# Optimization experiments

Hardware: AMD Instinct MI355X
Metric: run time of the kernel (lower is better)

Reference implementation:

```python
import jax, jax.numpy as jnp
import numpy as np

CONF_THRES = 0.25
IOU_THRES = 0.45
MAX_WH = 4096.0   # class offset for class-aware NMS (nc=1 -> offset is 0 anyway)
K = 1024          # fixed candidate pool (jit-friendly stand-in for max_nms)
MAX_DET = 300     # max detections per image (as in yolov5 NMS)


def xywh2xyxy(b):
    xy, wh = b[..., :2], b[..., 2:4]
    return jnp.concatenate([xy - wh * 0.5, xy + wh * 0.5], axis=-1)


def box_iou(a, b):
    # a: [K,4], b: [K,4] in xyxy -> [K,K] IoU
    area_a = (a[:, 2] - a[:, 0]) * (a[:, 3] - a[:, 1])
    area_b = (b[:, 2] - b[:, 0]) * (b[:, 3] - b[:, 1])
    lt = jnp.maximum(a[:, None, :2], b[None, :, :2])
    rb = jnp.minimum(a[:, None, 2:], b[None, :, 2:])
    wh = jnp.clip(rb - lt, 0.0)
    inter = wh[..., 0] * wh[..., 1]
    return inter / (area_a[:, None] + area_b[None, :] - inter + 1e-9)


def _nms_single(pred):
    # pred: [N, 6] = [xywh, obj_conf, cls_conf] (single class)
    boxes = xywh2xyxy(pred[:, :4])
    conf = pred[:, 4] * pred[:, 5]          # obj * cls  (nc=1 best-class path)
    cls = jnp.zeros_like(conf)              # single class -> class 0
    scores = jnp.where(conf > CONF_THRES, conf, -1.0)  # conf filter
    top_scores, idx = jax.lax.top_k(scores, K)          # candidates, sorted desc
    b = boxes[idx]
    c = cls[idx]
    bo = b + (c * MAX_WH)[:, None]          # class offset (no-op for nc=1)
    iou = box_iou(bo, bo)                   # [K, K]
    valid = top_scores > CONF_THRES

    def body(i, keep):
        sup = (iou[i] > IOU_THRES) & keep[i] & (jnp.arange(K) > i)
        return keep & ~sup

    keep = jax.lax.fori_loop(0, K, body, valid)  # greedy suppression
    keep_scores = jnp.where(keep, top_scores, -1.0)
    _, sel = jax.lax.top_k(keep_scores, MAX_DET)  # top MAX_DET kept, score order
    det = jnp.concatenate([b, top_scores[:, None], c[:, None]], axis=-1)[sel]
    det_valid = keep_scores[sel] > CONF_THRES
    return jnp.where(det_valid[:, None], det, 0.0)  # [MAX_DET, 6], zero-padded


def setup_inputs() -> dict:
    key = jax.random.key(0)
    k1, k2, k3, k4 = jax.random.split(key, 4)
    B, N = 32, 25200
    xy = jax.random.uniform(k1, (B, N, 2), jnp.float32) * 640.0
    wh = jax.random.uniform(k2, (B, N, 2), jnp.float32) * 160.0 + 4.0
    obj = jax.random.uniform(k3, (B, N, 1), jnp.float32)
    clsc = jax.random.uniform(k4, (B, N, 1), jnp.float32)
    x = jnp.concatenate([xy, wh, obj, clsc], axis=-1)  # [B, N, 6]
    return {"x": x}


def reference(x):
    # NMS.forward: non_max_suppression(x[0], conf_thres=0.25, iou_thres=0.45)
    return jax.vmap(_nms_single)(x)  # [B, MAX_DET, 6] (x1,y1,x2,y2,conf,cls)
```

## Files before the change

kernel.cpp:

```cpp
#include <hip/hip_runtime.h>
#include <stdint.h>

#define NBOX 25200
#define BATCH 32
#define TOPK 1024
#define MAXDET 300
#define BINCAP 2048
#define SEGCAP 256
#define NSEG 64
#define CONF_T 0.25f
#define IOU_T 0.45f
#define KEY_BIAS 0x3E800001u

#define SEGS_OFF   0u
#define SEGCNT_OFF 4194304u
#define GHIST_OFF  4202496u
#define SORTED_OFF 4726784u
#define SBOX_OFF   4988928u
#define SAREA_OFF  5513216u
#define MASKS_OFF  5644288u
#define WS_NEED    7741440u

__device__ __forceinline__ float iou_of(float4 a, float ar_a, float4 bq, float ar_b) {
    float xx1 = fmaxf(a.x, bq.x);
    float yy1 = fmaxf(a.y, bq.y);
    float xx2 = fminf(a.z, bq.z);
    float yy2 = fminf(a.w, bq.w);
    float iw = fmaxf(xx2 - xx1, 0.0f);
    float ih = fmaxf(yy2 - yy1, 0.0f);
    float inter = iw * ih;
    return inter / (ar_a + ar_b - inter + 1e-9f);
}

__global__ __launch_bounds__(256) void k1_extract(const float* __restrict__ x,
                                                  unsigned long long* __restrict__ segs,
                                                  unsigned* __restrict__ segcnt,
                                                  unsigned* __restrict__ ghist) {
    const int blk = blockIdx.x;
    const int b = blk >> 4;
    const int sl = blk & 15;
    const int tid = threadIdx.x;
    const int lane = tid & 63;
    const int wv = tid >> 6;
    const int seg = sl * 4 + wv;
    const float* __restrict__ xb = x + (size_t)b * NBOX * 6;
    unsigned long long* __restrict__ sb = segs + ((size_t)b * NSEG + seg) * SEGCAP;

    __shared__ unsigned hist[256];
    hist[tid] = 0;
    __syncthreads();

    const int n0 = (seg * NBOX) / NSEG;
    const int n1 = ((seg + 1) * NBOX) / NSEG;
    unsigned base = 0;
    const unsigned long long lmask = (1ull << lane) - 1ull;
    #pragma unroll 2
    for (int n = n0 + lane; n < n1; n += 64) {
        float2 oc = *reinterpret_cast<const float2*>(xb + n * 6 + 4);
        float conf = oc.x * oc.y;
        bool take = conf > CONF_T;
        unsigned key = 0;
        if (take) {
            key = __float_as_uint(conf) - KEY_BIAS;
            atomicAdd(&hist[min(key >> 16, 255u)], 1u);
        }
        unsigned long long m = __ballot(take);
        if (take) {
            unsigned pos = base + (unsigned)__popcll(m & lmask);
            if (pos < SEGCAP)
                sb[pos] = ((unsigned long long)key << 32) | (unsigned)(~(unsigned)n);
        }
        base += (unsigned)__popcll(m);
    }
    if (lane == 0) segcnt[b * NSEG + seg] = min(base, (unsigned)SEGCAP);
    __syncthreads();
    ghist[(size_t)blk * 256 + tid] = hist[tid];
}

__global__ __launch_bounds__(1024) void k2_sort(const float* __restrict__ x,
                                                const unsigned long long* __restrict__ segs,
                                                const unsigned* __restrict__ segcnt,
                                                const unsigned* __restrict__ ghist,
                                                unsigned long long* __restrict__ sorted_g,
                                                float4* __restrict__ sbox,
                                                float* __restrict__ sarea) {
    const int b = blockIdx.x;
    const int tid = threadIdx.x;
    const int lane = tid & 63;
    const float* __restrict__ xb = x + (size_t)b * NBOX * 6;
    const unsigned long long* __restrict__ segs_b = segs + (size_t)b * NSEG * SEGCAP;

    __shared__ unsigned hist[256];
    __shared__ unsigned binstart[256];
    __shared__ unsigned bincnt[256];
    __shared__ int sh_selbin;
    __shared__ unsigned segcnt_l[NSEG];
    __shared__ unsigned long long cand[BINCAP];
    __shared__ unsigned long long sortedl[TOPK];

    if (tid < 256) {
        unsigned h = 0;
        #pragma unroll
        for (int sl = 0; sl < 16; ++sl) h += ghist[((size_t)(b * 16 + sl)) * 256 + tid];
        hist[tid] = h;
        bincnt[tid] = 0;
    }
    if (tid < NSEG) segcnt_l[tid] = segcnt[b * NSEG + tid];
    if (tid == 0) sh_selbin = 0;
    sortedl[tid] = 0ull;
    __syncthreads();

    if (tid < 64) {
        unsigned c0 = hist[tid*4+0], c1 = hist[tid*4+1];
        unsigned c2 = hist[tid*4+2], c3 = hist[tid*4+3];
        unsigned s3 = c3, s2 = c2 + s3, s1 = c1 + s2, s0 = c0 + s1;
        unsigned suf = s0;
        #pragma unroll
        for (int off = 1; off < 64; off <<= 1) {
            unsigned o = (unsigned)__shfl_down((int)suf, off);
            if (lane + off < 64) suf += o;
        }
        unsigned excl = suf - s0;
        binstart[tid*4+0] = excl + s1;
        binstart[tid*4+1] = excl + s2;
        binstart[tid*4+2] = excl + s3;
        binstart[tid*4+3] = excl;
        unsigned S0 = excl+s0, S1 = excl+s1, S2 = excl+s2, S3 = excl+s3;
        if (S0 >= TOPK && S1 < TOPK) sh_selbin = tid*4+0;
        if (S1 >= TOPK && S2 < TOPK) sh_selbin = tid*4+1;
        if (S2 >= TOPK && S3 < TOPK) sh_selbin = tid*4+2;
        if (S3 >= TOPK && excl < TOPK) sh_selbin = tid*4+3;
    }
    __syncthreads();
    const unsigned selbin = (unsigned)sh_selbin;
    const int C = (int)min(binstart[selbin] + hist[selbin], (unsigned)BINCAP);

    for (int idx = tid; idx < NSEG * SEGCAP; idx += 1024) {
        const int seg = idx >> 8;
        const int i = idx & (SEGCAP - 1);
        if (i < (int)segcnt_l[seg]) {
            unsigned long long pk = segs_b[idx];
            unsigned bin = (unsigned)(pk >> 48);
            if (bin >= selbin) {
                unsigned pos = binstart[bin] + atomicAdd(&bincnt[bin], 1u);
                if (pos < BINCAP) cand[pos] = pk;
            }
        }
    }
    __syncthreads();

    for (int e = tid; e < C; e += 1024) {
        unsigned long long mine = cand[e];
        unsigned bin = (unsigned)(mine >> 48);
        unsigned js = binstart[bin];
        unsigned je = min(js + hist[bin], (unsigned)C);
        int rank = (int)js;
        for (unsigned j = js; j < je; ++j) rank += (cand[j] > mine) ? 1 : 0;
        if (rank < TOPK) sortedl[rank] = mine;
    }
    __syncthreads();

    unsigned long long pk = sortedl[tid];
    sorted_g[(size_t)b * TOPK + tid] = pk;
    int n = (int)(~(unsigned)pk);
    if (n < 0 || n >= NBOX) n = 0;
    float2 p01 = *reinterpret_cast<const float2*>(xb + n * 6);
    float2 p23 = *reinterpret_cast<const float2*>(xb + n * 6 + 2);
    float x1 = p01.x - p23.x * 0.5f, y1 = p01.y - p23.y * 0.5f;
    float x2 = p01.x + p23.x * 0.5f, y2 = p01.y + p23.y * 0.5f;
    sbox[(size_t)b * TOPK + tid] = make_float4(x1, y1, x2, y2);
    sarea[(size_t)b * TOPK + tid] = (x2 - x1) * (y2 - y1);
}

__global__ __launch_bounds__(256) void k3_masks(const float4* __restrict__ sbox,
                                                const float* __restrict__ sarea,
                                                unsigned long long* __restrict__ masks) {
    const int b = blockIdx.y;
    const int wv = threadIdx.x >> 6;
    const int j = threadIdx.x & 63;
    const int p = blockIdx.x * 4 + wv;

    int jc = (int)((sqrtf(8.0f * (float)p + 1.0f) - 1.0f) * 0.5f);
    while ((jc + 1) * (jc + 2) / 2 <= p) ++jc;
    while (jc * (jc + 1) / 2 > p) --jc;
    const int ic = p - jc * (jc + 1) / 2;

    __shared__ float4 ibox[4][64];
    __shared__ float iar[4][64];
    ibox[wv][j] = sbox[(size_t)b * TOPK + ic * 64 + j];
    iar[wv][j]  = sarea[(size_t)b * TOPK + ic * 64 + j];
    const float4 mb = sbox[(size_t)b * TOPK + jc * 64 + j];
    const float ma  = sarea[(size_t)b * TOPK + jc * 64 + j];
    __syncthreads();

    unsigned long long w = 0ull;
    #pragma unroll 4
    for (int i = 0; i < 64; ++i) {
        float iou = iou_of(ibox[wv][i], iar[wv][i], mb, ma);
        bool bit = (iou > IOU_T) && (ic != jc || i < j);
        if (bit) w |= (1ull << i);
    }
    masks[(((size_t)b * 16 + jc) * 16 + ic) * 64 + j] = w;
}

__global__ __launch_bounds__(1024) void k4_resolve(const unsigned long long* __restrict__ sorted_g,
                                                   const float4* __restrict__ sbox,
                                                   const unsigned long long* __restrict__ masks,
                                                   float* __restrict__ out) {
    const int b = blockIdx.x;
    const int tid = threadIdx.x;
    const int lane = tid & 63;
    const int wv = tid >> 6;

    __shared__ unsigned long long keptb[16];
    __shared__ int pre[17];
    __shared__ int sh_acc, sh_cut;

    if (tid < 16) keptb[tid] = 0ull;
    if (tid == 0) { sh_acc = 0; sh_cut = 15; }

    const unsigned long long pk = sorted_g[(size_t)b * TOPK + tid];
    bool alive = (pk != 0ull);

    unsigned long long wcs[16];
    #pragma unroll
    for (int c = 0; c < 16; ++c)
        wcs[c] = masks[(((size_t)b * 16 + wv) * 16 + c) * 64 + lane];

    #pragma unroll
    for (int c = 0; c < 16; ++c) {
        if (wv == c) {
            unsigned long long rem = __ballot(alive);
            unsigned long long kept = 0ull;
            while (rem) {
                int i = __ffsll((long long)rem) - 1;
                unsigned long long bit = 1ull << i;
                kept |= bit;
                unsigned long long row = __ballot((unsigned)((wcs[c] >> i) & 1ull));
                rem &= ~(row | bit);
            }
            alive = (kept >> lane) & 1ull;
            if (lane == 0) {
                keptb[c] = kept;
                int acc = sh_acc + (int)__popcll(kept);
                sh_acc = acc;
                if (acc >= MAXDET && c < sh_cut) sh_cut = c;
            }
        }
        __syncthreads();
        if (c >= sh_cut) break;
        if (wv > c && alive && (wcs[c] & keptb[c])) alive = false;
    }

    if (tid == 0) {
        int acc = 0;
        #pragma unroll
        for (int c = 0; c < 16; ++c) { pre[c] = acc; acc += (int)__popcll(keptb[c]); }
        pre[16] = acc;
    }
    __syncthreads();
    const int total = pre[16];

    float* __restrict__ ob = out + (size_t)b * MAXDET * 6;
    const int rank = pre[wv] + (int)__popcll(keptb[wv] & ((1ull << lane) - 1ull));
    if (alive && wv <= sh_cut && rank < MAXDET) {
        float4 bx = sbox[(size_t)b * TOPK + tid];
        float sc_ = __uint_as_float((unsigned)(pk >> 32) + KEY_BIAS);
        ob[rank * 6 + 0] = bx.x;
        ob[rank * 6 + 1] = bx.y;
        ob[rank * 6 + 2] = bx.z;
        ob[rank * 6 + 3] = bx.w;
        ob[rank * 6 + 4] = sc_;
        ob[rank * 6 + 5] = 0.0f;
    }
    for (int r = tid; r < MAXDET; r += 1024) {
        if (r >= total) {
            #pragma unroll
            for (int cc = 0; cc < 6; ++cc) ob[r * 6 + cc] = 0.0f;
        }
    }
}

__global__ __launch_bounds__(1024) void nms_single_kernel(const float* __restrict__ x,
                                                          float* __restrict__ out) {
    const int b = blockIdx.x;
    const int tid = threadIdx.x;
    const int lane = tid & 63;
    const int wv = tid >> 6;
    const float* __restrict__ xb = x + (size_t)b * NBOX * 6;

    __shared__ unsigned hist[256];
    __shared__ int sh_selbin;
    __shared__ unsigned sh_cnt;
    __shared__ unsigned long long cand[BINCAP];
    __shared__ unsigned long long keys[TOPK];
    __shared__ float4 bbox[TOPK];
    __shared__ float bar[TOPK];
    __shared__ float4 lbox[2][64];
    __shared__ float lar[2][64];
    __shared__ int listn[2];
    __shared__ int wcnt[16], wpre[16];
    __shared__ int sh_total;

    if (tid < 256) hist[tid] = 0;
    if (tid == 0) { sh_selbin = 0; sh_cnt = 0; }
    keys[tid] = 0ull;
    __syncthreads();
    for (int n = tid; n < NBOX; n += 1024) {
        float2 oc = *reinterpret_cast<const float2*>(xb + n * 6 + 4);
        float conf = oc.x * oc.y;
        if (conf > CONF_T) atomicAdd(&hist[(__float_as_uint(conf) - KEY_BIAS) >> 16], 1u);
    }
    __syncthreads();
    if (tid < 64) {
        unsigned c0 = hist[tid*4+0], c1 = hist[tid*4+1];
        unsigned c2 = hist[tid*4+2], c3 = hist[tid*4+3];
        unsigned s3 = c3, s2 = c2 + s3, s1 = c1 + s2, s0 = c0 + s1;
        unsigned suf = s0;
        #pragma unroll
        for (int off = 1; off < 64; off <<= 1) {
            unsigned o = (unsigned)__shfl_down((int)suf, off);
            if (lane + off < 64) suf += o;
        }
        unsigned excl = suf - s0;
        unsigned S0 = excl+s0, S1 = excl+s1, S2 = excl+s2, S3 = excl+s3;
        if (S0 >= TOPK && S1 < TOPK) sh_selbin = tid*4+0;
        if (S1 >= TOPK && S2 < TOPK) sh_selbin = tid*4+1;
        if (S2 >= TOPK && S3 < TOPK) sh_selbin = tid*4+2;
        if (S3 >= TOPK && excl < TOPK) sh_selbin = tid*4+3;
    }
    __syncthreads();
    const unsigned selbin = (unsigned)sh_selbin;
    for (int n = tid; n < NBOX; n += 1024) {
        float2 oc = *reinterpret_cast<const float2*>(xb + n * 6 + 4);
        float conf = oc.x * oc.y;
        bool take = false; unsigned key = 0;
        if (conf > CONF_T) {
            key = __float_as_uint(conf) - KEY_BIAS;
            take = ((key >> 16) >= selbin);
        }
        unsigned long long m = __ballot(take);
        unsigned base = 0;
        if (lane == 0 && m) base = atomicAdd(&sh_cnt, (unsigned)__popcll(m));
        base = (unsigned)__shfl((int)base, 0);
        if (take) {
            unsigned pos = base + (unsigned)__popcll(m & ((1ull << lane) - 1ull));
            if (pos < BINCAP)
                cand[pos] = ((unsigned long long)key << 32) | (unsigned)(~(unsigned)n);
        }
    }
    __syncthreads();
    const int C = (int)min(sh_cnt, (unsigned)BINCAP);
    for (int e = tid; e < C; e += 1024) {
        unsigned long long mine = cand[e];
        int rank = 0;
        #pragma unroll 8
        for (int j = 0; j < C; ++j) rank += (cand[j] > mine) ? 1 : 0;
        if (rank < TOPK) keys[rank] = mine;
    }
    __syncthreads();
    unsigned long long kk = keys[tid];
    unsigned key24 = (unsigned)(kk >> 32);
    int n = (int)(~(unsigned)kk);
    bool alive = (kk != 0ull);
    if (n < 0 || n >= NBOX) { n = 0; alive = false; }
    float sc_ = __uint_as_float(key24 + KEY_BIAS);
    float2 p01 = *reinterpret_cast<const float2*>(xb + n * 6);
    float2 p23 = *reinterpret_cast<const float2*>(xb + n * 6 + 2);
    float x1 = p01.x - p23.x * 0.5f, y1 = p01.y - p23.y * 0.5f;
    float x2 = p01.x + p23.x * 0.5f, y2 = p01.y + p23.y * 0.5f;
    float4 mybox = make_float4(x1, y1, x2, y2);
    float my_ar = (x2 - x1) * (y2 - y1);
    bbox[tid] = mybox;
    bar[tid] = my_ar;
    __syncthreads();
    const int cbase = tid & ~63;
    unsigned long long my_mask = 0ull;
    #pragma unroll 4
    for (int i = 0; i < 64; ++i) {
        float iou = iou_of(bbox[cbase + i], bar[cbase + i], mybox, my_ar);
        if (i < lane && iou > IOU_T) my_mask |= (1ull << i);
    }
    for (int c = 0; c < 16; ++c) {
        if (c > 0 && wv >= c && alive) {
            const int pb = (c - 1) & 1;
            const int m = listn[pb];
            bool sup = false;
            #pragma unroll 2
            for (int t = 0; t < m; ++t) {
                float iou = iou_of(lbox[pb][t], lar[pb][t], mybox, my_ar);
                sup = sup || (iou > IOU_T);
            }
            alive = !sup;
        }
        if (wv == c) {
            unsigned long long rem = __ballot(alive);
            unsigned long long kept = 0ull;
            while (rem) {
                int i = __ffsll((long long)rem) - 1;
                unsigned long long bit = 1ull << i;
                kept |= bit;
                unsigned long long row = __ballot((unsigned)((my_mask >> i) & 1ull));
                rem &= ~(row | bit);
            }
            alive = (kept >> lane) & 1ull;
            int nk = __popcll(kept);
            int rk = __popcll(kept & ((1ull << lane) - 1ull));
            if (alive) { lbox[c & 1][rk] = mybox; lar[c & 1][rk] = my_ar; }
            if (lane == 0) listn[c & 1] = nk;
        }
        __syncthreads();
    }
    unsigned long long m = __ballot(alive);
    if (lane == 0) wcnt[wv] = __popcll(m);
    __syncthreads();
    if (tid == 0) {
        int acc = 0;
        for (int w2 = 0; w2 < 16; ++w2) { wpre[w2] = acc; acc += wcnt[w2]; }
        sh_total = acc;
    }
    __syncthreads();
    const int rank = wpre[wv] + (int)__popcll(m & ((1ull << lane) - 1ull));
    const int total = sh_total;
    float* __restrict__ ob = out + (size_t)b * MAXDET * 6;
    if (alive && rank < MAXDET) {
        ob[rank * 6 + 0] = mybox.x;
        ob[rank * 6 + 1] = mybox.y;
        ob[rank * 6 + 2] = mybox.z;
        ob[rank * 6 + 3] = mybox.w;
        ob[rank * 6 + 4] = sc_;
        ob[rank * 6 + 5] = 0.0f;
    }
    for (int r = tid; r < MAXDET; r += 1024) {
        if (r >= total) {
            #pragma unroll
            for (int cc = 0; cc < 6; ++cc) ob[r * 6 + cc] = 0.0f;
        }
    }
}

extern "C" void kernel_launch(void* const* d_in, const int* in_sizes, int n_in,
                              void* d_out, int out_size, void* d_ws, size_t ws_size,
                              hipStream_t stream) {
    const float* x = (const float*)d_in[0];
    float* out = (float*)d_out;
    if (ws_size >= (size_t)WS_NEED) {
        char* ws = (char*)d_ws;
        unsigned long long* segs   = (unsigned long long*)(ws + SEGS_OFF);
        unsigned* segcnt           = (unsigned*)(ws + SEGCNT_OFF);
        unsigned* ghist            = (unsigned*)(ws + GHIST_OFF);
        unsigned long long* sorted = (unsigned long long*)(ws + SORTED_OFF);
        float4* sbox               = (float4*)(ws + SBOX_OFF);
        float* sarea               = (float*)(ws + SAREA_OFF);
        unsigned long long* masks  = (unsigned long long*)(ws + MASKS_OFF);
        hipLaunchKernelGGL(k1_extract, dim3(512), dim3(256), 0, stream,
                           x, segs, segcnt, ghist);
        hipLaunchKernelGGL(k2_sort, dim3(BATCH), dim3(1024), 0, stream,
                           x, segs, segcnt, ghist, sorted, sbox, sarea);
        hipLaunchKernelGGL(k3_masks, dim3(34, BATCH), dim3(256), 0, stream,
                           sbox, sarea, masks);
        hipLaunchKernelGGL(k4_resolve, dim3(BATCH), dim3(1024), 0, stream,
                           sorted, sbox, masks, out);
    } else {
        hipLaunchKernelGGL(nms_single_kernel, dim3(BATCH), dim3(1024), 0, stream, x, out);
    }
}
```

Measured before the change: 57.58 us.

## Split per-image top-K sort across four blocks by histogram bin quarter

```diff
diff --git a/kernel.cpp b/kernel.cpp
--- a/kernel.cpp
+++ b/kernel.cpp
@@ -84,7 +84,8 @@
                                                 unsigned long long* __restrict__ sorted_g,
                                                 float4* __restrict__ sbox,
                                                 float* __restrict__ sarea) {
-    const int b = blockIdx.x;
+    const int q = blockIdx.x;
+    const int b = blockIdx.y;
     const int tid = threadIdx.x;
     const int lane = tid & 63;
     const float* __restrict__ xb = x + (size_t)b * NBOX * 6;
@@ -92,22 +93,23 @@
 
     __shared__ unsigned hist[256];
     __shared__ unsigned binstart[256];
-    __shared__ unsigned bincnt[256];
+    __shared__ unsigned bincnt[64];
     __shared__ int sh_selbin;
     __shared__ unsigned segcnt_l[NSEG];
     __shared__ unsigned long long cand[BINCAP];
-    __shared__ unsigned long long sortedl[TOPK];
+    __shared__ unsigned long long sortedl[BINCAP];
 
     if (tid < 256) {
         unsigned h = 0;
         #pragma unroll
         for (int sl = 0; sl < 16; ++sl) h += ghist[((size_t)(b * 16 + sl)) * 256 + tid];
         hist[tid] = h;
-        bincnt[tid] = 0;
-    }
+    }
+    if (tid < 64) bincnt[tid] = 0;
     if (tid < NSEG) segcnt_l[tid] = segcnt[b * NSEG + tid];
     if (tid == 0) sh_selbin = 0;
     sortedl[tid] = 0ull;
+    sortedl[tid + 1024] = 0ull;
     __syncthreads();
 
     if (tid < 64) {
@@ -132,8 +134,11 @@
         if (S3 >= TOPK && excl < TOPK) sh_selbin = tid*4+3;
     }
     __syncthreads();
-    const unsigned selbin = (unsigned)sh_selbin;
-    const int C = (int)min(binstart[selbin] + hist[selbin], (unsigned)BINCAP);
+    const int selbin = sh_selbin;
+    const unsigned C = min(binstart[selbin] + hist[selbin], (unsigned)BINCAP);
+    const unsigned lo  = binstart[q * 64 + 63];
+    const unsigned hiq = binstart[q * 64] + hist[q * 64];
+    const unsigned myC = min(hiq, C);
 
     for (int idx = tid; idx < NSEG * SEGCAP; idx += 1024) {
         const int seg = idx >> 8;
@@ -141,35 +146,40 @@
         if (i < (int)segcnt_l[seg]) {
             unsigned long long pk = segs_b[idx];
             unsigned bin = (unsigned)(pk >> 48);
-            if (bin >= selbin) {
-                unsigned pos = binstart[bin] + atomicAdd(&bincnt[bin], 1u);
-                if (pos < BINCAP) cand[pos] = pk;
+            if ((int)bin >= selbin && (bin >> 6) == (unsigned)q) {
+                unsigned pos = binstart[bin] + atomicAdd(&bincnt[bin & 63], 1u);
+                if (pos < BINCAP) cand[pos - lo] = pk;
             }
         }
     }
     __syncthreads();
 
-    for (int e = tid; e < C; e += 1024) {
+    const int nloc = (int)myC - (int)lo;
+    for (int e = tid; e < nloc; e += 1024) {
         unsigned long long mine = cand[e];
         unsigned bin = (unsigned)(mine >> 48);
         unsigned js = binstart[bin];
-        unsigned je = min(js + hist[bin], (unsigned)C);
+        unsigned je = min(js + hist[bin], C);
         int rank = (int)js;
-        for (unsigned j = js; j < je; ++j) rank += (cand[j] > mine) ? 1 : 0;
-        if (rank < TOPK) sortedl[rank] = mine;
-    }
-    __syncthreads();
-
-    unsigned long long pk = sortedl[tid];
-    sorted_g[(size_t)b * TOPK + tid] = pk;
-    int n = (int)(~(unsigned)pk);
-    if (n < 0 || n >= NBOX) n = 0;
-    float2 p01 = *reinterpret_cast<const float2*>(xb + n * 6);
-    float2 p23 = *reinterpret_cast<const float2*>(xb + n * 6 + 2);
-    float x1 = p01.x - p23.x * 0.5f, y1 = p01.y - p23.y * 0.5f;
-    float x2 = p01.x + p23.x * 0.5f, y2 = p01.y + p23.y * 0.5f;
-    sbox[(size_t)b * TOPK + tid] = make_float4(x1, y1, x2, y2);
-    sarea[(size_t)b * TOPK + tid] = (x2 - x1) * (y2 - y1);
+        for (unsigned j = js; j < je; ++j) rank += (cand[j - lo] > mine) ? 1 : 0;
+        if (rank < TOPK) sortedl[rank - lo] = mine;
+    }
+    __syncthreads();
+
+    unsigned wend = min(myC, (unsigned)TOPK);
+    if (q == 0 && selbin == 0) wend = TOPK;
+    for (unsigned p = lo + tid; p < wend; p += 1024) {
+        unsigned long long pk = sortedl[p - lo];
+        sorted_g[(size_t)b * TOPK + p] = pk;
+        int n = (int)(~(unsigned)pk);
+        if (n < 0 || n >= NBOX) n = 0;
+        float2 p01 = *reinterpret_cast<const float2*>(xb + n * 6);
+        float2 p23 = *reinterpret_cast<const float2*>(xb + n * 6 + 2);
+        float x1 = p01.x - p23.x * 0.5f, y1 = p01.y - p23.y * 0.5f;
+        float x2 = p01.x + p23.x * 0.5f, y2 = p01.y + p23.y * 0.5f;
+        sbox[(size_t)b * TOPK + p] = make_float4(x1, y1, x2, y2);
+        sarea[(size_t)b * TOPK + p] = (x2 - x1) * (y2 - y1);
+    }
 }
 
 __global__ __launch_bounds__(256) void k3_masks(const float4* __restrict__ sbox,
@@ -455,7 +465,7 @@
         unsigned long long* masks  = (unsigned long long*)(ws + MASKS_OFF);
         hipLaunchKernelGGL(k1_extract, dim3(512), dim3(256), 0, stream,
                            x, segs, segcnt, ghist);
-        hipLaunchKernelGGL(k2_sort, dim3(BATCH), dim3(1024), 0, stream,
+        hipLaunchKernelGGL(k2_sort, dim3(4, BATCH), dim3(1024), 0, stream,
                            x, segs, segcnt, ghist, sorted, sbox, sarea);
         hipLaunchKernelGGL(k3_masks, dim3(34, BATCH), dim3(256), 0, stream,
                            sbox, sarea, masks);
```

Measured after the change: 58.60 us. No clear change (+1.8%).

## Process box pairs in extract and halve resolve block with lazy mask loads

Applied to the files above, without the earlier changes.

```diff
diff --git a/kernel.cpp b/kernel.cpp
--- a/kernel.cpp
+++ b/kernel.cpp
@@ -8,6 +8,7 @@
 #define BINCAP 2048
 #define SEGCAP 256
 #define NSEG 64
+#define SEGSZ 394
 #define CONF_T 0.25f
 #define IOU_T 0.45f
 #define KEY_BIAS 0x3E800001u
@@ -50,27 +51,40 @@
     hist[tid] = 0;
     __syncthreads();
 
-    const int n0 = (seg * NBOX) / NSEG;
-    const int n1 = ((seg + 1) * NBOX) / NSEG;
+    const int n0 = seg * SEGSZ;
+    const int n1 = min(n0 + SEGSZ, NBOX);
     unsigned base = 0;
     const unsigned long long lmask = (1ull << lane) - 1ull;
-    #pragma unroll 2
-    for (int n = n0 + lane; n < n1; n += 64) {
-        float2 oc = *reinterpret_cast<const float2*>(xb + n * 6 + 4);
-        float conf = oc.x * oc.y;
-        bool take = conf > CONF_T;
-        unsigned key = 0;
-        if (take) {
-            key = __float_as_uint(conf) - KEY_BIAS;
-            atomicAdd(&hist[min(key >> 16, 255u)], 1u);
-        }
-        unsigned long long m = __ballot(take);
-        if (take) {
-            unsigned pos = base + (unsigned)__popcll(m & lmask);
+    for (int n = n0 + 2 * lane; n < n1; n += 128) {
+        const float4 B = *reinterpret_cast<const float4*>(xb + n * 6 + 4);
+        const float4 Cv = *reinterpret_cast<const float4*>(xb + n * 6 + 8);
+        float conf0 = B.x * B.y;
+        float conf1 = Cv.z * Cv.w;
+        bool take0 = conf0 > CONF_T;
+        bool take1 = conf1 > CONF_T;
+        unsigned key0 = 0, key1 = 0;
+        if (take0) {
+            key0 = __float_as_uint(conf0) - KEY_BIAS;
+            atomicAdd(&hist[min(key0 >> 16, 255u)], 1u);
+        }
+        if (take1) {
+            key1 = __float_as_uint(conf1) - KEY_BIAS;
+            atomicAdd(&hist[min(key1 >> 16, 255u)], 1u);
+        }
+        unsigned long long m0 = __ballot(take0);
+        if (take0) {
+            unsigned pos = base + (unsigned)__popcll(m0 & lmask);
             if (pos < SEGCAP)
-                sb[pos] = ((unsigned long long)key << 32) | (unsigned)(~(unsigned)n);
-        }
-        base += (unsigned)__popcll(m);
+                sb[pos] = ((unsigned long long)key0 << 32) | (unsigned)(~(unsigned)n);
+        }
+        base += (unsigned)__popcll(m0);
+        unsigned long long m1 = __ballot(take1);
+        if (take1) {
+            unsigned pos = base + (unsigned)__popcll(m1 & lmask);
+            if (pos < SEGCAP)
+                sb[pos] = ((unsigned long long)key1 << 32) | (unsigned)(~(unsigned)(n + 1));
+        }
+        base += (unsigned)__popcll(m1);
     }
     if (lane == 0) segcnt[b * NSEG + seg] = min(base, (unsigned)SEGCAP);
     __syncthreads();
@@ -203,10 +217,10 @@
     masks[(((size_t)b * 16 + jc) * 16 + ic) * 64 + j] = w;
 }
 
-__global__ __launch_bounds__(1024) void k4_resolve(const unsigned long long* __restrict__ sorted_g,
-                                                   const float4* __restrict__ sbox,
-                                                   const unsigned long long* __restrict__ masks,
-                                                   float* __restrict__ out) {
+__global__ __launch_bounds__(512) void k4_resolve(const unsigned long long* __restrict__ sorted_g,
+                                                  const float4* __restrict__ sbox,
+                                                  const unsigned long long* __restrict__ masks,
+                                                  float* __restrict__ out) {
     const int b = blockIdx.x;
     const int tid = threadIdx.x;
     const int lane = tid & 63;
@@ -219,27 +233,28 @@
     if (tid < 16) keptb[tid] = 0ull;
     if (tid == 0) { sh_acc = 0; sh_cut = 15; }
 
-    const unsigned long long pk = sorted_g[(size_t)b * TOPK + tid];
-    bool alive = (pk != 0ull);
-
-    unsigned long long wcs[16];
-    #pragma unroll
-    for (int c = 0; c < 16; ++c)
-        wcs[c] = masks[(((size_t)b * 16 + wv) * 16 + c) * 64 + lane];
-
-    #pragma unroll
+    const int cA = 2 * wv, cB = 2 * wv + 1;
+    const unsigned long long pkA = sorted_g[(size_t)b * TOPK + cA * 64 + lane];
+    const unsigned long long pkB = sorted_g[(size_t)b * TOPK + cB * 64 + lane];
+    bool aA = (pkA != 0ull), aB = (pkB != 0ull);
+    const unsigned long long* __restrict__ mk = masks + (size_t)b * 16 * 16 * 64;
+    __syncthreads();
+
     for (int c = 0; c < 16; ++c) {
-        if (wv == c) {
-            unsigned long long rem = __ballot(alive);
+        if (wv == (c >> 1)) {
+            const unsigned long long diag = mk[((size_t)c * 16 + c) * 64 + lane];
+            bool al = (c & 1) ? aB : aA;
+            unsigned long long rem = __ballot(al);
             unsigned long long kept = 0ull;
             while (rem) {
                 int i = __ffsll((long long)rem) - 1;
                 unsigned long long bit = 1ull << i;
                 kept |= bit;
-                unsigned long long row = __ballot((unsigned)((wcs[c] >> i) & 1ull));
+                unsigned long long row = __ballot((unsigned)((diag >> i) & 1ull));
                 rem &= ~(row | bit);
             }
-            alive = (kept >> lane) & 1ull;
+            al = (kept >> lane) & 1ull;
+            if (c & 1) aB = al; else aA = al;
             if (lane == 0) {
                 keptb[c] = kept;
                 int acc = sh_acc + (int)__popcll(kept);
@@ -249,7 +264,15 @@
         }
         __syncthreads();
         if (c >= sh_cut) break;
-        if (wv > c && alive && (wcs[c] & keptb[c])) alive = false;
+        const unsigned long long kc = keptb[c];
+        if (cA > c && aA) {
+            unsigned long long m = mk[((size_t)cA * 16 + c) * 64 + lane];
+            if (m & kc) aA = false;
+        }
+        if (cB > c && aB) {
+            unsigned long long m = mk[((size_t)cB * 16 + c) * 64 + lane];
+            if (m & kc) aB = false;
+        }
     }
 
     if (tid == 0) {
@@ -260,20 +283,29 @@
     }
     __syncthreads();
     const int total = pre[16];
+    const int cut = sh_cut;
 
     float* __restrict__ ob = out + (size_t)b * MAXDET * 6;
-    const int rank = pre[wv] + (int)__popcll(keptb[wv] & ((1ull << lane) - 1ull));
-    if (alive && wv <= sh_cut && rank < MAXDET) {
-        float4 bx = sbox[(size_t)b * TOPK + tid];
-        float sc_ = __uint_as_float((unsigned)(pk >> 32) + KEY_BIAS);
-        ob[rank * 6 + 0] = bx.x;
-        ob[rank * 6 + 1] = bx.y;
-        ob[rank * 6 + 2] = bx.z;
-        ob[rank * 6 + 3] = bx.w;
-        ob[rank * 6 + 4] = sc_;
-        ob[rank * 6 + 5] = 0.0f;
-    }
-    for (int r = tid; r < MAXDET; r += 1024) {
+    const unsigned long long lm = (1ull << lane) - 1ull;
+    if (aA && cA <= cut) {
+        int rank = pre[cA] + (int)__popcll(keptb[cA] & lm);
+        if (rank < MAXDET) {
+            float4 bx = sbox[(size_t)b * TOPK + cA * 64 + lane];
+            float sc = __uint_as_float((unsigned)(pkA >> 32) + KEY_BIAS);
+            ob[rank*6+0] = bx.x; ob[rank*6+1] = bx.y; ob[rank*6+2] = bx.z;
+            ob[rank*6+3] = bx.w; ob[rank*6+4] = sc;   ob[rank*6+5] = 0.0f;
+        }
+    }
+    if (aB && cB <= cut) {
+        int rank = pre[cB] + (int)__popcll(keptb[cB] & lm);
+        if (rank < MAXDET) {
+            float4 bx = sbox[(size_t)b * TOPK + cB * 64 + lane];
+            float sc = __uint_as_float((unsigned)(pkB >> 32) + KEY_BIAS);
+            ob[rank*6+0] = bx.x; ob[rank*6+1] = bx.y; ob[rank*6+2] = bx.z;
+            ob[rank*6+3] = bx.w; ob[rank*6+4] = sc;   ob[rank*6+5] = 0.0f;
+        }
+    }
+    for (int r = tid; r < MAXDET; r += 512) {
         if (r >= total) {
             #pragma unroll
             for (int cc = 0; cc < 6; ++cc) ob[r * 6 + cc] = 0.0f;
@@ -459,7 +491,7 @@
                            x, segs, segcnt, ghist, sorted, sbox, sarea);
         hipLaunchKernelGGL(k3_masks, dim3(34, BATCH), dim3(256), 0, stream,
                            sbox, sarea, masks);
-        hipLaunchKernelGGL(k4_resolve, dim3(BATCH), dim3(1024), 0, stream,
+        hipLaunchKernelGGL(k4_resolve, dim3(BATCH), dim3(512), 0, stream,
                            sorted, sbox, masks, out);
     } else {
         hipLaunchKernelGGL(nms_single_kernel, dim3(BATCH), dim3(1024), 0, stream, x, out);
```

Result: slower. 62.55 us (+8.6%).
